# Optimization experiments

Hardware: AMD Instinct MI355X
Metric: run time of the kernel (lower is better)

Reference implementation:

```python
import jax, jax.numpy as jnp
from jax import lax
import numpy as np

KSIZE = 3        # matching kernel size
RATE = 2         # downsample rate; raw kernel = 2*RATE = 4
FUSE_K = 3       # fusion (diagonal-sum) kernel size
SOFTMAX_SCALE = 10.0
EPS = 1e-4


def extract_patches(x, k, s, pad):
    """im2col: x [B,C,H,W] -> patches [B, L, C, k, k], L = oH*oW (row-major),
    matching torch.nn.Unfold ordering after the view/permute in the source."""
    B, C, H, W = x.shape
    xp = jnp.pad(x, ((0, 0), (0, 0), (pad, pad), (pad, pad)))
    Hp, Wp = H + 2 * pad, W + 2 * pad
    oH = (Hp - k) // s + 1
    oW = (Wp - k) // s + 1
    cols = []
    for i in range(k):
        for j in range(k):
            cols.append(xp[:, :, i:i + (oH - 1) * s + 1:s, j:j + (oW - 1) * s + 1:s])
    p = jnp.stack(cols, axis=0).reshape(k, k, B, C, oH, oW)
    return p.transpose(2, 4, 5, 3, 0, 1).reshape(B, oH * oW, C, k, k)


def fuse_diag(y, k):
    """conv2d with identity (eye(k)) kernel, 'same' padding == sum of diagonal shifts."""
    r = k // 2
    n0, n1 = y.shape
    yp = jnp.pad(y, r)
    return sum(yp[r + d:r + d + n0, r + d:r + d + n1] for d in range(-r, r + 1))


def _per_sample(xi, wi, raw_wi, mi):
    # xi: [C,Hs,Ws] downsampled foreground; wi: [L,C,3,3] bg patches;
    # raw_wi: [L,C,4,4] raw bg patches; mi: [L] patch validity mask
    C, Hs, Ws = xi.shape
    L = wi.shape[0]
    # L2-normalize each background patch (EPS added per-element inside the sum, as in source)
    wi_norm = jnp.sqrt(jnp.sum(wi * wi + EPS, axis=(1, 2, 3), keepdims=True))
    wn = (wi / wi_norm).reshape(L, -1)                      # [L, C*9]
    # correlation scores: conv2d(xi, wi_normed, pad=1) expressed as a GEMM over im2col patches
    fp = extract_patches(xi[None], KSIZE, 1, KSIZE // 2)[0].reshape(L, -1)  # [L_f, C*9]
    yi = wn @ fp.T                                          # [L_b, L_f]
    # fusion trick: identity-kernel conv along both diagonal orientations
    yi = fuse_diag(yi, FUSE_K)
    yi = yi.reshape(Hs, Ws, Hs, Ws).transpose(1, 0, 3, 2).reshape(L, L)
    yi = fuse_diag(yi, FUSE_K)
    yi = yi.reshape(Ws, Hs, Ws, Hs).transpose(1, 0, 3, 2)
    yi = yi.reshape(L, Hs, Ws)
    m = mi[:, None, None]
    yi = jax.nn.softmax(yi * m * SOFTMAX_SCALE, axis=0) * m  # softmax over bg-patch axis
    # transposed conv reconstruction with raw 4x4 patches, stride=RATE, padding=1
    k = 2 * RATE
    w_t = jnp.flip(raw_wi, (2, 3)).transpose(1, 0, 2, 3)     # [C, L, 4, 4] OIHW
    out = lax.conv_general_dilated(
        yi[None], w_t, window_strides=(1, 1),
        padding=[(k - 1 - 1, k - 1 - 1)] * 2, lhs_dilation=(RATE, RATE),
        dimension_numbers=('NCHW', 'OIHW', 'NCHW'))[0] / 4.0  # [C, H, W]
    return out


def setup_inputs() -> dict:
    key = jax.random.key(0)
    k1, k2 = jax.random.split(key)
    B, C, H, W = 4, 128, 96, 96
    b = jax.random.normal(k1, (B, C, H, W), jnp.float32)
    f = jax.random.normal(k2, (B, C, H, W), jnp.float32)
    mask = jnp.ones((B, 1, H, W), jnp.float32)
    return {"b": b, "f": f, "mask": mask}


def reference(b, f, mask):
    B, C, H, W = b.shape
    k_raw = 2 * RATE
    # raw patches from full-res background: k=4, stride=2, pad=1 (get_pad 'valid')
    raw_w = extract_patches(b, k_raw, RATE, 1)               # [B, L, C, 4, 4]
    # nearest downsample by RATE (F.interpolate nearest, scale 1/rate)
    fs = f[:, :, ::RATE, ::RATE]
    bs = b[:, :, ::RATE, ::RATE]
    Hs, Ws = fs.shape[2], fs.shape[3]
    w = extract_patches(bs, KSIZE, 1, KSIZE // 2)            # [B, L, C, 3, 3]
    ms = mask.shape[3] // Ws
    m_small = mask[:, :, ::ms, ::ms]                         # [B, 1, Hs, Ws]
    m = extract_patches(m_small, KSIZE, 1, KSIZE // 2)       # [B, L, 1, 3, 3]
    mm = (jnp.mean(m, axis=(2, 3, 4)) == 1.0).astype(jnp.float32)  # [B, L]
    y = jax.vmap(_per_sample)(fs, w, raw_w, mm)              # [B, C, H, W]
    return y
```

## Files before the change

### kernel.cpp

```cpp
#include <hip/hip_runtime.h>
#include <hip/hip_bf16.h>
#include <math.h>

#define NS   4
#define CH   128
#define HW   96
#define GS   48
#define LL   2304
#define CKN  2048
#define SCALE 10.0f
#define EPSSUM 0.1152f
#define PCH2 32
#define NCH2 72

#define S_IN  ((size_t)CH * HW * HW)
#define S_MK  ((size_t)HW * HW)
#define S_PM  ((size_t)NCH2 * LL)
#define S_BUF ((size_t)LL * LL)
#define S_W2  ((size_t)CKN * LL)
#define S_AT  ((size_t)LL * LL)

typedef __attribute__((ext_vector_type(8))) short short8;
typedef __attribute__((ext_vector_type(4))) float float4v;

#define GLDS16(gptr, lptr) \
    __builtin_amdgcn_global_load_lds((const __attribute__((address_space(1))) void*)(gptr), \
        (__attribute__((address_space(3))) void*)(lptr), 16, 0, 0)

__device__ __forceinline__ float4 ld4(const float* p) { return *reinterpret_cast<const float4*>(p); }

__global__ __launch_bounds__(256) void k_stage_split(const float* __restrict__ b, const float* __restrict__ f,
                                                     float* __restrict__ ssq, float* __restrict__ bufB) {
    __shared__ float tile[32][33];
    int z = blockIdx.z;
    int s = z >> 1, sel = z & 1;
    const float* X = (sel ? f : b) + s * S_IN;
    __hip_bfloat16* base = (__hip_bfloat16*)(bufB + s * S_BUF);
    __hip_bfloat16* hi = base + (size_t)sel * 2 * LL * CH;
    __hip_bfloat16* lo = hi + (size_t)LL * CH;
    int r0 = blockIdx.x * 32, c0 = blockIdx.y * 32;
    int tx = threadIdx.x & 31, ty = threadIdx.x >> 5;

#pragma unroll
    for (int j = 0; j < 4; ++j) {
        int c  = c0 + ty + 8 * j;
        int rs = r0 + tx;
        int r = rs / GS, ss_ = rs % GS;
        tile[ty + 8 * j][tx] = X[(size_t)c * HW * HW + (2 * r) * HW + 2 * ss_];
    }
    __syncthreads();

    if (sel == 0 && ty == 0) {
        float acc = 0.f;
        for (int cl = 0; cl < 32; ++cl) { float v = tile[cl][tx]; acc += v * v; }
        atomicAdd(&ssq[(size_t)s * LL + r0 + tx], acc);
    }

#pragma unroll
    for (int j = 0; j < 4; ++j) {
        int rl = ty + 8 * j, cl = tx;
        float v = tile[cl][rl];
        __hip_bfloat16 h = __float2bfloat16(v);
        float resid = v - __bfloat162float(h);
        hi[(size_t)(r0 + rl) * CH + c0 + cl] = h;
        lo[(size_t)(r0 + rl) * CH + c0 + cl] = __float2bfloat16(resid);
    }
}

__global__ __launch_bounds__(256) void k_norm_mm(const float* __restrict__ ssq, const float* __restrict__ mk,
                                                 float* __restrict__ invn, float* __restrict__ mmv) {
    int sI = blockIdx.z;
    ssq += (size_t)sI * LL; mk += sI * S_MK; invn += (size_t)sI * LL; mmv += (size_t)sI * LL;
    int p = blockIdx.x * 256 + threadIdx.x;
    int ph = p / GS, pw = p % GS;
    float acc = EPSSUM;
    float msum = 0.f;
    for (int di = -1; di <= 1; ++di)
        for (int dj = -1; dj <= 1; ++dj) {
            int r = ph + di, s = pw + dj;
            if (r >= 0 && r < GS && s >= 0 && s < GS) {
                acc  += ssq[r * GS + s];
                msum += mk[(2 * r) * HW + 2 * s];
            }
        }
    invn[p] = 1.0f / sqrtf(acc);
    mmv[p]  = (msum / 9.0f == 1.0f) ? 1.0f : 0.0f;
}

__global__ __launch_bounds__(256) void k_w2T(const float* __restrict__ b, __hip_bfloat16* __restrict__ W2T) {
    int sI = blockIdx.z;
    b += sI * S_IN; W2T += sI * S_W2;
    int ck = blockIdx.y;
    int p  = blockIdx.x * 256 + threadIdx.x;
    int c = ck >> 4, dy = (ck >> 2) & 3, dx = ck & 3;
    int ph = p / GS, pw = p % GS;
    int r = 2 * ph + dy - 1, s = 2 * pw + dx - 1;
    float v = 0.f;
    if (r >= 0 && r < HW && s >= 0 && s < HW) v = b[c * HW * HW + r * HW + s];
    W2T[(size_t)ck * LL + p] = __float2bfloat16(v);
}

__global__ __launch_bounds__(256) void gemm1_mfma(const float* __restrict__ bufB, float* __restrict__ bufA) {
    __shared__ __hip_bfloat16 sAh[128 * 32];
    __shared__ __hip_bfloat16 sAl[128 * 32];
    __shared__ __hip_bfloat16 sBh[128 * 32];
    __shared__ __hip_bfloat16 sBl[128 * 32];
    int sI = blockIdx.z;
    const __hip_bfloat16* base = (const __hip_bfloat16*)(bufB + sI * S_BUF);
    const __hip_bfloat16* Ahi = base;
    const __hip_bfloat16* Alo = Ahi + (size_t)LL * CH;
    const __hip_bfloat16* Bhi = Alo + (size_t)LL * CH;
    const __hip_bfloat16* Blo = Bhi + (size_t)LL * CH;
    float* C = bufA + sI * S_BUF;

    int t = threadIdx.x, lane = t & 63, w = t >> 6;
    int wr = w >> 1, wc = w & 1;
    int m0 = blockIdx.y * 128, n0 = blockIdx.x * 128;

    float4v acc[4][4];
#pragma unroll
    for (int i = 0; i < 4; ++i)
#pragma unroll
        for (int j = 0; j < 4; ++j) acc[i][j] = (float4v){0.f, 0.f, 0.f, 0.f};

    for (int k0 = 0; k0 < 128; k0 += 32) {
#pragma unroll
        for (int it = 0; it < 2; ++it) {
            int chunk = it * 256 + w * 64 + lane;
            int row = chunk >> 2, ps = chunk & 3;
            int pd = ps ^ (row & 3);
            size_t ga = (size_t)(m0 + row) * 128 + k0 + pd * 8;
            size_t gb = (size_t)(n0 + row) * 128 + k0 + pd * 8;
            GLDS16(Ahi + ga, (char*)sAh + (size_t)chunk * 16);
            GLDS16(Alo + ga, (char*)sAl + (size_t)chunk * 16);
            GLDS16(Bhi + gb, (char*)sBh + (size_t)chunk * 16);
            GLDS16(Blo + gb, (char*)sBl + (size_t)chunk * 16);
        }
        __syncthreads();

        int lrow = lane & 15, part = lane >> 4;
        int sw = part ^ (lrow & 3);
        short8 ah[4], al[4], bh[4], bl[4];
#pragma unroll
        for (int i = 0; i < 4; ++i) {
            int slot = (wr * 64 + i * 16 + lrow) * 4 + sw;
            ah[i] = *reinterpret_cast<const short8*>(sAh + (size_t)slot * 8);
            al[i] = *reinterpret_cast<const short8*>(sAl + (size_t)slot * 8);
        }
#pragma unroll
        for (int j = 0; j < 4; ++j) {
            int slot = (wc * 64 + j * 16 + lrow) * 4 + sw;
            bh[j] = *reinterpret_cast<const short8*>(sBh + (size_t)slot * 8);
            bl[j] = *reinterpret_cast<const short8*>(sBl + (size_t)slot * 8);
        }
#pragma unroll
        for (int i = 0; i < 4; ++i)
#pragma unroll
            for (int j = 0; j < 4; ++j) {
                acc[i][j] = __builtin_amdgcn_mfma_f32_16x16x32_bf16(ah[i], bh[j], acc[i][j], 0, 0, 0);
                acc[i][j] = __builtin_amdgcn_mfma_f32_16x16x32_bf16(ah[i], bl[j], acc[i][j], 0, 0, 0);
                acc[i][j] = __builtin_amdgcn_mfma_f32_16x16x32_bf16(al[i], bh[j], acc[i][j], 0, 0, 0);
            }
        __syncthreads();
    }

    int col = lane & 15, rbase = (lane >> 4) * 4;
#pragma unroll
    for (int i = 0; i < 4; ++i)
#pragma unroll
        for (int j = 0; j < 4; ++j)
#pragma unroll
            for (int r = 0; r < 4; ++r) {
                int m = m0 + wr * 64 + i * 16 + rbase + r;
                int n = n0 + wc * 64 + j * 16 + col;
                C[(size_t)m * LL + n] = acc[i][j][r];
            }
}

__global__ __launch_bounds__(256) void gemm2_mfma(const __hip_bfloat16* __restrict__ W2T_,
                                                  const __hip_bfloat16* __restrict__ attnT_,
                                                  float* __restrict__ bufA) {
    __shared__ __hip_bfloat16 As[128 * 32];
    __shared__ __hip_bfloat16 Bs[128 * 32];
    int sI = blockIdx.z;
    const __hip_bfloat16* A = W2T_ + sI * S_W2;
    const __hip_bfloat16* B = attnT_ + sI * S_AT;
    __hip_bfloat16* C = (__hip_bfloat16*)(bufA + sI * S_BUF);

    int t = threadIdx.x;
    int lane = t & 63, w = t >> 6;
    int wr = w >> 1, wc = w & 1;

    int flat = blockIdx.y * 18 + blockIdx.x;
    int swz  = (flat & 7) * 36 + (flat >> 3);
    int by = swz / 18, bx = swz % 18;
    int m0 = by * 128, n0 = bx * 128;

    float4v acc[4][4];
#pragma unroll
    for (int i = 0; i < 4; ++i)
#pragma unroll
        for (int j = 0; j < 4; ++j) acc[i][j] = (float4v){0.f, 0.f, 0.f, 0.f};

    for (int k0 = 0; k0 < LL; k0 += 32) {
#pragma unroll
        for (int it = 0; it < 2; ++it) {
            int chunk = it * 256 + w * 64 + lane;
            int row = chunk >> 2, ps = chunk & 3;
            int pd = ps ^ (row & 3);
            const __hip_bfloat16* ga = A + (size_t)(m0 + row) * LL + k0 + pd * 8;
            const __hip_bfloat16* gb = B + (size_t)(n0 + row) * LL + k0 + pd * 8;
            GLDS16(ga, (char*)As + (size_t)chunk * 16);
            GLDS16(gb, (char*)Bs + (size_t)chunk * 16);
        }
        __syncthreads();

        int lrow = lane & 15, part = lane >> 4;
        int sw = part ^ (lrow & 3);
        short8 afrag[4], bfrag[4];
#pragma unroll
        for (int i = 0; i < 4; ++i) {
            int slot = (wr * 64 + i * 16 + lrow) * 4 + sw;
            afrag[i] = *reinterpret_cast<const short8*>(As + (size_t)slot * 8);
        }
#pragma unroll
        for (int j = 0; j < 4; ++j) {
            int slot = (wc * 64 + j * 16 + lrow) * 4 + sw;
            bfrag[j] = *reinterpret_cast<const short8*>(Bs + (size_t)slot * 8);
        }
#pragma unroll
        for (int i = 0; i < 4; ++i)
#pragma unroll
            for (int j = 0; j < 4; ++j)
                acc[i][j] = __builtin_amdgcn_mfma_f32_16x16x32_bf16(afrag[i], bfrag[j], acc[i][j], 0, 0, 0);
        __syncthreads();
    }

    int col = lane & 15, rbase = (lane >> 4) * 4;
#pragma unroll
    for (int i = 0; i < 4; ++i)
#pragma unroll
        for (int j = 0; j < 4; ++j)
#pragma unroll
            for (int r = 0; r < 4; ++r) {
                int m = m0 + wr * 64 + i * 16 + rbase + r;
                int n = n0 + wc * 64 + j * 16 + col;
                C[(size_t)m * LL + n] = __float2bfloat16(acc[i][j][r]);
            }
}

__global__ __launch_bounds__(192) void k_corr_v4(const float* __restrict__ bufA, const float* __restrict__ invn,
                                                 float* __restrict__ bufB) {
    int sI = blockIdx.z;
    const float* D = bufA + sI * S_BUF;
    float* yi = bufB + sI * S_BUF;
    invn += (size_t)sI * LL;

    int p  = blockIdx.y;
    int qi = blockIdx.x * 192 + threadIdx.x;
    int q4 = qi * 4;
    int qh = q4 / GS, qw0 = q4 % GS;
    int ph = p / GS, pw = p % GS;

    float4 acc = {0.f, 0.f, 0.f, 0.f};
#pragma unroll
    for (int di = -1; di <= 1; ++di) {
        int rp = ph + di, tq = qh + di;
        if (rp < 0 || rp >= GS || tq < 0 || tq >= GS) continue;
        int r0 = rp * GS + pw;
        int c0 = tq * GS + qw0;
        {
            float4 Cc = ld4(D + (size_t)r0 * LL + c0);
            acc.x += Cc.x; acc.y += Cc.y; acc.z += Cc.z; acc.w += Cc.w;
        }
        if (pw > 0) {
            const float* rowm = D + (size_t)(r0 - 1) * LL;
            float4 L  = ld4(rowm + (qw0 > 0 ? c0 - 4 : c0));
            float4 Cm = ld4(rowm + c0);
            acc.x += (qw0 > 0 ? L.w : 0.f);
            acc.y += Cm.x; acc.z += Cm.y; acc.w += Cm.z;
        }
        if (pw < GS - 1) {
            const float* rowp = D + (size_t)(r0 + 1) * LL;
            float4 Cp = ld4(rowp + c0);
            float4 R  = ld4(rowp + (qw0 < GS - 4 ? c0 + 4 : c0));
            acc.x += Cp.y; acc.y += Cp.z; acc.z += Cp.w;
            acc.w += (qw0 < GS - 4 ? R.x : 0.f);
        }
    }
    float inv = invn[p];
    float4 outv = {inv * acc.x, inv * acc.y, inv * acc.z, inv * acc.w};
    *reinterpret_cast<float4*>(yi + (size_t)p * LL + q4) = outv;
}

__global__ __launch_bounds__(192) void k_fuse1_v4(const float* __restrict__ bufB, float* __restrict__ bufA) {
    int sI = blockIdx.z;
    const float* yi = bufB + sI * S_BUF;
    float* S1 = bufA + sI * S_BUF;
    int a  = blockIdx.y;
    int bi = blockIdx.x * 192 + threadIdx.x;
    int b4 = bi * 4;

    float4 acc = ld4(yi + (size_t)a * LL + b4);
    if (a > 0) {
        const float* rowm = yi + (size_t)(a - 1) * LL;
        float4 L  = ld4(rowm + (b4 > 0 ? b4 - 4 : b4));
        float4 Cm = ld4(rowm + b4);
        acc.x += (b4 > 0 ? L.w : 0.f);
        acc.y += Cm.x; acc.z += Cm.y; acc.w += Cm.z;
    }
    if (a < LL - 1) {
        const float* rowp = yi + (size_t)(a + 1) * LL;
        float4 Cp = ld4(rowp + b4);
        float4 R  = ld4(rowp + (b4 < LL - 4 ? b4 + 4 : b4));
        acc.x += Cp.y; acc.y += Cp.z; acc.z += Cp.w;
        acc.w += (b4 < LL - 4 ? R.x : 0.f);
    }
    *reinterpret_cast<float4*>(S1 + (size_t)a * LL + b4) = acc;
}

__device__ __forceinline__ int gmap(int x) { int hi = x / GS; int lo = x - hi * GS; return lo * GS + hi; }

__global__ __launch_bounds__(192) void k_fuse2_sm_v4(const float* __restrict__ bufA, const float* __restrict__ mmv,
                                                     float* __restrict__ bufB,
                                                     float* __restrict__ pmax, float* __restrict__ psum) {
    int sI = blockIdx.z;
    const float* S1 = bufA + sI * S_BUF;
    float* S2 = bufB + sI * S_BUF;
    mmv += (size_t)sI * LL; pmax += sI * S_PM; psum += sI * S_PM;
    int qi = blockIdx.x * 192 + threadIdx.x;
    int q4 = qi * 4;
    int qh = q4 / GS, qw0 = q4 % GS;
    int p0 = blockIdx.y * PCH2;
    float mxa[4], sma[4];
#pragma unroll
    for (int j = 0; j < 4; ++j) { mxa[j] = -1e30f; sma[j] = 0.f; }

    for (int i = 0; i < PCH2; ++i) {
        int p = p0 + i;
        int ph = p / GS, pw = p % GS;
        int a0 = pw * GS + ph;
        float sarr[4] = {0.f, 0.f, 0.f, 0.f};
#pragma unroll
        for (int e = -1; e <= 1; ++e) {
            int ae = a0 + e;
            if (ae < 0 || ae >= LL) continue;
            int Ar = gmap(ae);
            const float* Rw = S1 + (size_t)Ar * LL;
            int qe = qh + e;
            if (qe >= 0 && qe < GS) {
                float4 v = ld4(Rw + q4 + 48 * e);
                sarr[0] += v.x; sarr[1] += v.y; sarr[2] += v.z; sarr[3] += v.w;
            } else {
#pragma unroll
                for (int j = 0; j < 4; ++j) {
                    int be = (qw0 + j) * GS + qh + e;
                    if (be >= 0 && be < LL) {
                        int bh = be / GS, bw = be % GS;
                        sarr[j] += Rw[bw * GS + bh];
                    }
                }
            }
        }
        float4 sv = {sarr[0], sarr[1], sarr[2], sarr[3]};
        *reinterpret_cast<float4*>(S2 + (size_t)p * LL + q4) = sv;
        float mv = mmv[p];
#pragma unroll
        for (int j = 0; j < 4; ++j) {
            float lg = (mv != 0.f) ? SCALE * sarr[j] : 0.f;
            float nm = fmaxf(mxa[j], lg);
            sma[j] = sma[j] * __expf(mxa[j] - nm) + __expf(lg - nm);
            mxa[j] = nm;
        }
    }
    float4 mo = {mxa[0], mxa[1], mxa[2], mxa[3]};
    float4 so = {sma[0], sma[1], sma[2], sma[3]};
    *reinterpret_cast<float4*>(pmax + blockIdx.y * LL + q4) = mo;
    *reinterpret_cast<float4*>(psum + blockIdx.y * LL + q4) = so;
}

__global__ __launch_bounds__(256) void k_sm2(const float* __restrict__ pmax, const float* __restrict__ psum,
                                             float* __restrict__ Mq, float* __restrict__ Dq) {
    __shared__ float red[4][64];
    int sI = blockIdx.z;
    pmax += sI * S_PM; psum += sI * S_PM; Mq += (size_t)sI * LL; Dq += (size_t)sI * LL;
    int t = threadIdx.x;
    int ql = t & 63, g = t >> 6;
    int q = blockIdx.x * 64 + ql;
    float mx = -1e30f;
    for (int ch = g * 18; ch < g * 18 + 18; ++ch) mx = fmaxf(mx, pmax[(size_t)ch * LL + q]);
    red[g][ql] = mx;
    __syncthreads();
    float mall = fmaxf(fmaxf(red[0][ql], red[1][ql]), fmaxf(red[2][ql], red[3][ql]));
    float sm = 0.f;
    for (int ch = g * 18; ch < g * 18 + 18; ++ch)
        sm += psum[(size_t)ch * LL + q] * __expf(pmax[(size_t)ch * LL + q] - mall);
    __syncthreads();
    red[g][ql] = sm;
    __syncthreads();
    if (g == 0) {
        Mq[q] = mall;
        Dq[q] = (red[0][ql] + red[1][ql]) + (red[2][ql] + red[3][ql]);
    }
}

__global__ __launch_bounds__(256) void k_sm3T(const float* __restrict__ bufB, const float* __restrict__ mmv,
                                              const float* __restrict__ Mq, const float* __restrict__ Dq,
                                              __hip_bfloat16* __restrict__ attnT) {
    __shared__ float tile[32][33];
    int sI = blockIdx.z;
    const float* S2 = bufB + sI * S_BUF;
    mmv += (size_t)sI * LL; Mq += (size_t)sI * LL; Dq += (size_t)sI * LL; attnT += sI * S_AT;
    int tx = threadIdx.x & 31, ty = threadIdx.x >> 5;
    int p0 = blockIdx.y * 32, q0 = blockIdx.x * 32;
    int q = q0 + tx;
    float mq = Mq[q], dq = Dq[q];
#pragma unroll
    for (int j = 0; j < 4; ++j) {
        int p = p0 + ty + 8 * j;
        float v = S2[(size_t)p * LL + q];
        float attn = (mmv[p] != 0.f) ? __expf(SCALE * v - mq) / dq : 0.f;
        tile[ty + 8 * j][tx] = attn;
    }
    __syncthreads();
#pragma unroll
    for (int j = 0; j < 4; ++j) {
        int qq = q0 + ty + 8 * j;
        attnT[(size_t)qq * LL + p0 + tx] = __float2bfloat16(tile[tx][ty + 8 * j]);
    }
}

__global__ __launch_bounds__(256) void k_out(const float* __restrict__ bufA, float* __restrict__ out) {
    int sI = blockIdx.z;
    const __hip_bfloat16* Z = (const __hip_bfloat16*)(bufA + sI * S_BUF);
    out += sI * S_IN;
    int c  = blockIdx.y;
    int yx = blockIdx.x * 256 + threadIdx.x;
    int y = yx / HW, x = yx % HW;
    int u = y >> 1, a = y & 1, v = x >> 1, w = x & 1;
    int qh1 = u + a - 1, qh2 = u + a, qw1 = v + w - 1, qw2 = v + w;
    int cb = c * 16;
    float s = 0.f;
    if (qh1 >= 0) {
        if (qw1 >= 0)  s += __bfloat162float(Z[(size_t)(cb + (3 - a) * 4 + (3 - w)) * LL + qh1 * GS + qw1]);
        if (qw2 < GS)  s += __bfloat162float(Z[(size_t)(cb + (3 - a) * 4 + (1 - w)) * LL + qh1 * GS + qw2]);
    }
    if (qh2 < GS) {
        if (qw1 >= 0)  s += __bfloat162float(Z[(size_t)(cb + (1 - a) * 4 + (3 - w)) * LL + qh2 * GS + qw1]);
        if (qw2 < GS)  s += __bfloat162float(Z[(size_t)(cb + (1 - a) * 4 + (1 - w)) * LL + qh2 * GS + qw2]);
    }
    out[(size_t)c * HW * HW + yx] = 0.25f * s;
}


extern "C" void kernel_launch(void* const* d_in, const int* in_sizes, int n_in,
                              void* d_out, int out_size, void* d_ws, size_t ws_size,
                              hipStream_t stream) {
    const float* b_all = (const float*)d_in[0];
    const float* f_all = (const float*)d_in[1];
    const float* m_all = (const float*)d_in[2];
    float* out = (float*)d_out;
    float* ws  = (float*)d_ws;

    const size_t perF = 5 * (size_t)LL + 2 * S_PM + 2 * S_BUF + S_W2 / 2 + S_AT / 2;
    const size_t perB = perF * sizeof(float);
    int nb = (ws_size >= NS * perB) ? NS : ((ws_size >= 2 * perB) ? 2 : 1);

    size_t off = 0;
    float* ssq  = ws + off; off += nb * (size_t)LL;
    float* invn = ws + off; off += nb * (size_t)LL;
    float* mmv  = ws + off; off += nb * (size_t)LL;
    float* Mq   = ws + off; off += nb * (size_t)LL;
    float* Dq   = ws + off; off += nb * (size_t)LL;
    float* pmax = ws + off; off += nb * S_PM;
    float* psum = ws + off; off += nb * S_PM;
    float* bufA = ws + off; off += nb * S_BUF;
    float* bufB = ws + off; off += nb * S_BUF;
    __hip_bfloat16* W2T   = (__hip_bfloat16*)(ws + off); off += nb * S_W2 / 2;
    __hip_bfloat16* attnT = (__hip_bfloat16*)(ws + off); off += nb * S_AT / 2;

    for (int s0 = 0; s0 < NS; s0 += nb) {
        const float* b  = b_all + s0 * S_IN;
        const float* f  = f_all + s0 * S_IN;
        const float* mk = m_all + s0 * S_MK;
        float* outp = out + s0 * S_IN;

        hipMemsetAsync(ssq, 0, nb * LL * sizeof(float), stream);
        k_stage_split<<<dim3(72, 4, 2 * nb), 256, 0, stream>>>(b, f, ssq, bufB);
        k_norm_mm    <<<dim3(9, 1, nb), 256, 0, stream>>>(ssq, mk, invn, mmv);
        k_w2T        <<<dim3(9, CKN, nb), 256, 0, stream>>>(b, W2T);

        gemm1_mfma   <<<dim3(18, 18, nb), 256, 0, stream>>>(bufB, bufA);
        k_corr_v4    <<<dim3(3, LL, nb), 192, 0, stream>>>(bufA, invn, bufB);
        k_fuse1_v4   <<<dim3(3, LL, nb), 192, 0, stream>>>(bufB, bufA);
        k_fuse2_sm_v4<<<dim3(3, NCH2, nb), 192, 0, stream>>>(bufA, mmv, bufB, pmax, psum);

        k_sm2      <<<dim3(36, 1, nb), 256, 0, stream>>>(pmax, psum, Mq, Dq);
        k_sm3T     <<<dim3(72, 72, nb), 256, 0, stream>>>(bufB, mmv, Mq, Dq, attnT);

        gemm2_mfma <<<dim3(LL / 128, CKN / 128, nb), 256, 0, stream>>>(W2T, attnT, bufA);
        k_out      <<<dim3(36, CH, nb), 256, 0, stream>>>(bufA, outp);
    }
}
```

Measured before the change: 522.8 us.

## Fuse small prep and softmax-reduction kernels to cut launches and memset

The atomic channel-group sum of squares becomes per-group partial writes, so the memset is no longer needed, and the norm/mask computation is folded into the W2T gather kernel. The softmax column max/sum reduction (k_sm2) is merged into the transpose/normalize kernel, so every tile block recomputes the column statistics from the 72 partials. This removes three launches and one memset per batch, but adds redundant reads of the pmax/psum partials across the 72 row-blocks.

```diff
diff --git a/kernel.cpp b/kernel.cpp
--- a/kernel.cpp
+++ b/kernel.cpp
@@ -30,7 +30,7 @@
 __device__ __forceinline__ float4 ld4(const float* p) { return *reinterpret_cast<const float4*>(p); }
 
 __global__ __launch_bounds__(256) void k_stage_split(const float* __restrict__ b, const float* __restrict__ f,
-                                                     float* __restrict__ ssq, float* __restrict__ bufB) {
+                                                     float* __restrict__ ssq4, float* __restrict__ bufB) {
     __shared__ float tile[32][33];
     int z = blockIdx.z;
     int s = z >> 1, sel = z & 1;
@@ -53,7 +53,7 @@
     if (sel == 0 && ty == 0) {
         float acc = 0.f;
         for (int cl = 0; cl < 32; ++cl) { float v = tile[cl][tx]; acc += v * v; }
-        atomicAdd(&ssq[(size_t)s * LL + r0 + tx], acc);
+        ssq4[(size_t)s * 4 * LL + (size_t)blockIdx.y * LL + r0 + tx] = acc;
     }
 
 #pragma unroll
@@ -67,37 +67,44 @@
     }
 }
 
-__global__ __launch_bounds__(256) void k_norm_mm(const float* __restrict__ ssq, const float* __restrict__ mk,
-                                                 float* __restrict__ invn, float* __restrict__ mmv) {
-    int sI = blockIdx.z;
-    ssq += (size_t)sI * LL; mk += sI * S_MK; invn += (size_t)sI * LL; mmv += (size_t)sI * LL;
-    int p = blockIdx.x * 256 + threadIdx.x;
-    int ph = p / GS, pw = p % GS;
-    float acc = EPSSUM;
-    float msum = 0.f;
-    for (int di = -1; di <= 1; ++di)
-        for (int dj = -1; dj <= 1; ++dj) {
-            int r = ph + di, s = pw + dj;
-            if (r >= 0 && r < GS && s >= 0 && s < GS) {
-                acc  += ssq[r * GS + s];
-                msum += mk[(2 * r) * HW + 2 * s];
+__global__ __launch_bounds__(256) void k_w2T_norm(const float* __restrict__ b, const float* __restrict__ mk,
+                                                  const float* __restrict__ ssq4,
+                                                  float* __restrict__ invn, float* __restrict__ mmv,
+                                                  __hip_bfloat16* __restrict__ W2T) {
+    int sI = blockIdx.z;
+    {
+        const float* bb = b + sI * S_IN;
+        __hip_bfloat16* W = W2T + sI * S_W2;
+        int ck = blockIdx.y;
+        int p  = blockIdx.x * 256 + threadIdx.x;
+        int c = ck >> 4, dy = (ck >> 2) & 3, dx = ck & 3;
+        int ph = p / GS, pw = p % GS;
+        int r = 2 * ph + dy - 1, s = 2 * pw + dx - 1;
+        float v = 0.f;
+        if (r >= 0 && r < HW && s >= 0 && s < HW) v = bb[c * HW * HW + r * HW + s];
+        W[(size_t)ck * LL + p] = __float2bfloat16(v);
+    }
+    if (blockIdx.y == 0) {
+        const float* sq = ssq4 + (size_t)sI * 4 * LL;
+        const float* m  = mk + sI * S_MK;
+        float* iv = invn + (size_t)sI * LL;
+        float* mv = mmv + (size_t)sI * LL;
+        int p = blockIdx.x * 256 + threadIdx.x;
+        int ph = p / GS, pw = p % GS;
+        float acc = EPSSUM;
+        float msum = 0.f;
+        for (int di = -1; di <= 1; ++di)
+            for (int dj = -1; dj <= 1; ++dj) {
+                int r = ph + di, s = pw + dj;
+                if (r >= 0 && r < GS && s >= 0 && s < GS) {
+                    int idx = r * GS + s;
+                    acc  += sq[idx] + sq[LL + idx] + sq[2 * LL + idx] + sq[3 * LL + idx];
+                    msum += m[(2 * r) * HW + 2 * s];
+                }
             }
-        }
-    invn[p] = 1.0f / sqrtf(acc);
-    mmv[p]  = (msum / 9.0f == 1.0f) ? 1.0f : 0.0f;
-}
-
-__global__ __launch_bounds__(256) void k_w2T(const float* __restrict__ b, __hip_bfloat16* __restrict__ W2T) {
-    int sI = blockIdx.z;
-    b += sI * S_IN; W2T += sI * S_W2;
-    int ck = blockIdx.y;
-    int p  = blockIdx.x * 256 + threadIdx.x;
-    int c = ck >> 4, dy = (ck >> 2) & 3, dx = ck & 3;
-    int ph = p / GS, pw = p % GS;
-    int r = 2 * ph + dy - 1, s = 2 * pw + dx - 1;
-    float v = 0.f;
-    if (r >= 0 && r < HW && s >= 0 && s < HW) v = b[c * HW * HW + r * HW + s];
-    W2T[(size_t)ck * LL + p] = __float2bfloat16(v);
+        iv[p] = 1.0f / sqrtf(acc);
+        mv[p] = (msum / 9.0f == 1.0f) ? 1.0f : 0.0f;
+    }
 }
 
 __global__ __launch_bounds__(256) void gemm1_mfma(const float* __restrict__ bufB, float* __restrict__ bufA) {
@@ -379,42 +386,38 @@
     *reinterpret_cast<float4*>(psum + blockIdx.y * LL + q4) = so;
 }
 
-__global__ __launch_bounds__(256) void k_sm2(const float* __restrict__ pmax, const float* __restrict__ psum,
-                                             float* __restrict__ Mq, float* __restrict__ Dq) {
-    __shared__ float red[4][64];
-    int sI = blockIdx.z;
-    pmax += sI * S_PM; psum += sI * S_PM; Mq += (size_t)sI * LL; Dq += (size_t)sI * LL;
+__global__ __launch_bounds__(256) void k_sm3T_full(const float* __restrict__ bufB, const float* __restrict__ mmv,
+                                                   const float* __restrict__ pmax, const float* __restrict__ psum,
+                                                   __hip_bfloat16* __restrict__ attnT) {
+    __shared__ float tile[32][33];
+    __shared__ float redM[8][32];
+    __shared__ float redS[8][32];
+    int sI = blockIdx.z;
+    const float* S2 = bufB + sI * S_BUF;
+    mmv += (size_t)sI * LL; pmax += sI * S_PM; psum += sI * S_PM; attnT += sI * S_AT;
     int t = threadIdx.x;
-    int ql = t & 63, g = t >> 6;
-    int q = blockIdx.x * 64 + ql;
-    float mx = -1e30f;
-    for (int ch = g * 18; ch < g * 18 + 18; ++ch) mx = fmaxf(mx, pmax[(size_t)ch * LL + q]);
-    red[g][ql] = mx;
-    __syncthreads();
-    float mall = fmaxf(fmaxf(red[0][ql], red[1][ql]), fmaxf(red[2][ql], red[3][ql]));
-    float sm = 0.f;
-    for (int ch = g * 18; ch < g * 18 + 18; ++ch)
-        sm += psum[(size_t)ch * LL + q] * __expf(pmax[(size_t)ch * LL + q] - mall);
-    __syncthreads();
-    red[g][ql] = sm;
-    __syncthreads();
-    if (g == 0) {
-        Mq[q] = mall;
-        Dq[q] = (red[0][ql] + red[1][ql]) + (red[2][ql] + red[3][ql]);
-    }
-}
-
-__global__ __launch_bounds__(256) void k_sm3T(const float* __restrict__ bufB, const float* __restrict__ mmv,
-                                              const float* __restrict__ Mq, const float* __restrict__ Dq,
-                                              __hip_bfloat16* __restrict__ attnT) {
-    __shared__ float tile[32][33];
-    int sI = blockIdx.z;
-    const float* S2 = bufB + sI * S_BUF;
-    mmv += (size_t)sI * LL; Mq += (size_t)sI * LL; Dq += (size_t)sI * LL; attnT += sI * S_AT;
-    int tx = threadIdx.x & 31, ty = threadIdx.x >> 5;
+    int tx = t & 31, ty = t >> 5;
     int p0 = blockIdx.y * 32, q0 = blockIdx.x * 32;
     int q = q0 + tx;
-    float mq = Mq[q], dq = Dq[q];
+
+    float mx = -1e30f;
+    for (int ch = ty * 9; ch < ty * 9 + 9; ++ch)
+        mx = fmaxf(mx, pmax[(size_t)ch * LL + q]);
+    redM[ty][tx] = mx;
+    __syncthreads();
+    float mall = redM[0][tx];
+#pragma unroll
+    for (int g = 1; g < 8; ++g) mall = fmaxf(mall, redM[g][tx]);
+    float sm = 0.f;
+    for (int ch = ty * 9; ch < ty * 9 + 9; ++ch)
+        sm += psum[(size_t)ch * LL + q] * __expf(pmax[(size_t)ch * LL + q] - mall);
+    redS[ty][tx] = sm;
+    __syncthreads();
+    float dall = redS[0][tx];
+#pragma unroll
+    for (int g = 1; g < 8; ++g) dall += redS[g][tx];
+
+    float mq = mall, dq = dall;
 #pragma unroll
     for (int j = 0; j < 4; ++j) {
         int p = p0 + ty + 8 * j;
@@ -462,16 +465,14 @@
     float* out = (float*)d_out;
     float* ws  = (float*)d_ws;
 
-    const size_t perF = 5 * (size_t)LL + 2 * S_PM + 2 * S_BUF + S_W2 / 2 + S_AT / 2;
+    const size_t perF = 6 * (size_t)LL + 2 * S_PM + 2 * S_BUF + S_W2 / 2 + S_AT / 2;
     const size_t perB = perF * sizeof(float);
     int nb = (ws_size >= NS * perB) ? NS : ((ws_size >= 2 * perB) ? 2 : 1);
 
     size_t off = 0;
-    float* ssq  = ws + off; off += nb * (size_t)LL;
+    float* ssq4 = ws + off; off += nb * 4 * (size_t)LL;
     float* invn = ws + off; off += nb * (size_t)LL;
     float* mmv  = ws + off; off += nb * (size_t)LL;
-    float* Mq   = ws + off; off += nb * (size_t)LL;
-    float* Dq   = ws + off; off += nb * (size_t)LL;
     float* pmax = ws + off; off += nb * S_PM;
     float* psum = ws + off; off += nb * S_PM;
     float* bufA = ws + off; off += nb * S_BUF;
@@ -485,20 +486,17 @@
         const float* mk = m_all + s0 * S_MK;
         float* outp = out + s0 * S_IN;
 
-        hipMemsetAsync(ssq, 0, nb * LL * sizeof(float), stream);
-        k_stage_split<<<dim3(72, 4, 2 * nb), 256, 0, stream>>>(b, f, ssq, bufB);
-        k_norm_mm    <<<dim3(9, 1, nb), 256, 0, stream>>>(ssq, mk, invn, mmv);
-        k_w2T        <<<dim3(9, CKN, nb), 256, 0, stream>>>(b, W2T);
+        k_stage_split<<<dim3(72, 4, 2 * nb), 256, 0, stream>>>(b, f, ssq4, bufB);
+        k_w2T_norm   <<<dim3(9, CKN, nb), 256, 0, stream>>>(b, mk, ssq4, invn, mmv, W2T);
 
         gemm1_mfma   <<<dim3(18, 18, nb), 256, 0, stream>>>(bufB, bufA);
         k_corr_v4    <<<dim3(3, LL, nb), 192, 0, stream>>>(bufA, invn, bufB);
         k_fuse1_v4   <<<dim3(3, LL, nb), 192, 0, stream>>>(bufB, bufA);
         k_fuse2_sm_v4<<<dim3(3, NCH2, nb), 192, 0, stream>>>(bufA, mmv, bufB, pmax, psum);
 
-        k_sm2      <<<dim3(36, 1, nb), 256, 0, stream>>>(pmax, psum, Mq, Dq);
-        k_sm3T     <<<dim3(72, 72, nb), 256, 0, stream>>>(bufB, mmv, Mq, Dq, attnT);
-
-        gemm2_mfma <<<dim3(LL / 128, CKN / 128, nb), 256, 0, stream>>>(W2T, attnT, bufA);
-        k_out      <<<dim3(36, CH, nb), 256, 0, stream>>>(bufA, outp);
-    }
-}
+        k_sm3T_full  <<<dim3(72, 72, nb), 256, 0, stream>>>(bufB, mmv, pmax, psum, attnT);
+
+        gemm2_mfma   <<<dim3(LL / 128, CKN / 128, nb), 256, 0, stream>>>(W2T, attnT, bufA);
+        k_out        <<<dim3(36, CH, nb), 256, 0, stream>>>(bufA, outp);
+    }
+}
```

Result: no change. 520.0 us (-0.5%).
